# Kernel tuning notes

Measured on AMD Instinct MI355X. Metric: run time of the kernel, lower is better.

## Reference

```python
import jax, jax.numpy as jnp
import numpy as np

N_TOKENS = 131072      # flattened batch of latents
EMBED_DIM = 64         # embedding_dim
NUM_CODES = 1024       # num_embeddings
COMMIT_COST = 0.25     # commitment_cost
EPS_NORM = 1e-12       # F.normalize eps


def _l2_normalize(x):
    # matches F.normalize(x, dim=1): x / max(||x||_2, eps)
    n = jnp.sqrt(jnp.sum(x * x, axis=1, keepdims=True))
    return x / jnp.maximum(n, EPS_NORM)


def setup_inputs() -> dict:
    key = jax.random.key(0)
    k_in, k_w = jax.random.split(key)
    inputs = jax.random.normal(k_in, (N_TOKENS, EMBED_DIM), dtype=jnp.float32)
    # codebook init: uniform(-1/K, 1/K), as in the torch module
    weight = jax.random.uniform(k_w, (NUM_CODES, EMBED_DIM), dtype=jnp.float32,
                                minval=-1.0 / NUM_CODES, maxval=1.0 / NUM_CODES)
    return {"inputs": inputs, "weight": weight}


def reference(inputs, weight):
    # Eval-mode forward of VectorQuantizer (EMA/anchor update is a training-only
    # in-place buffer mutation and is excluded from the functional reference).
    input_shape = inputs.shape
    d = weight.shape[1]
    flat = inputs.reshape(-1, d)                         # [N, D]

    normed_z = _l2_normalize(jax.lax.stop_gradient(flat))  # [N, D]
    normed_cb = _l2_normalize(weight)                       # [K, D]
    # distances = -cosine similarity; argmin picks closest code
    distances = -jnp.einsum('nd,kd->nk', normed_z, normed_cb)  # [N, K]
    idx = jnp.argmin(distances, axis=1)                         # [N]

    encodings = jax.nn.one_hot(idx, weight.shape[0], dtype=jnp.float32)  # [N, K]
    # one-hot @ weight == gather of codebook rows
    quantized = jnp.take(weight, idx, axis=0).reshape(input_shape)

    e_latent_loss = jnp.mean((jax.lax.stop_gradient(quantized) - inputs) ** 2)
    q_latent_loss = jnp.mean((quantized - jax.lax.stop_gradient(inputs)) ** 2)
    loss = q_latent_loss + COMMIT_COST * e_latent_loss

    # straight-through estimator
    quantized_st = inputs + jax.lax.stop_gradient(quantized - inputs)

    avg_probs = jnp.mean(encodings, axis=0)  # [K]
    perplexity = jnp.exp(-jnp.sum(avg_probs * jnp.log(avg_probs + 1e-10)))

    return loss, quantized_st, perplexity, encodings
```

## Files before the change

### kernel.cpp

```cpp
#include <hip/hip_runtime.h>
#include <math.h>

#define N_TOK 131072
#define DIM 64
#define KCODES 1024
#define TPB 128
#define TIE_EPS 1e-4f

typedef __attribute__((ext_vector_type(8))) short short8;
typedef __attribute__((ext_vector_type(4))) float float4v;

static __device__ inline unsigned short f2bf(float x) {
    unsigned u = __float_as_uint(x);
    unsigned r = (u + 0x7FFF + ((u >> 16) & 1)) >> 16;
    return (unsigned short)r;
}
static __device__ inline float bf2f(unsigned short b) {
    return __uint_as_float(((unsigned)b) << 16);
}

__global__ __launch_bounds__(64) void vq_prep(
    const float* __restrict__ w, unsigned short* __restrict__ bfrag_hi,
    unsigned short* __restrict__ bfrag_lo, double* __restrict__ inv_n64,
    float* __restrict__ nw, int* __restrict__ count, int* __restrict__ nflag,
    double* __restrict__ delta)
{
    int k = blockIdx.x;
    int d = threadIdx.x;
    float v = w[k * DIM + d];
    float s = v * v;
    #pragma unroll
    for (int off = 32; off; off >>= 1) s += __shfl_xor(s, off);
    float den = fmaxf(sqrtf(s), 1e-12f);
    float nv = v / den;
    unsigned short hi = f2bf(nv);
    unsigned short lo = f2bf(nv - bf2f(hi));

    int t  = k >> 4;
    int nl = k & 15;
    int s2 = d >> 5;
    int q  = (d >> 3) & 3;
    int j  = d & 7;
    int l  = nl + 16 * q;
    size_t pos = ((size_t)(t * 2 + s2) * 64 + l) * 8 + j;
    bfrag_hi[pos] = hi;
    bfrag_lo[pos] = lo;

    double vd = (double)v;
    double sd = vd * vd;
    #pragma unroll
    for (int off = 32; off; off >>= 1) sd += __shfl_xor(sd, off);
    if (d == 0) {
        inv_n64[k] = 1.0 / fmax(sqrt(sd), 1e-12);
        nw[k] = den;
    }
    if (k == 0) {
        for (int i = d; i < KCODES; i += 64) count[i] = 0;
        if (d == 0) { nflag[0] = 0; delta[0] = 0.0; }
    }
}

static __device__ inline void merge3(float& b, float& s, int& i, float ob, float os, int oi) {
    if (ob > b) { s = fmaxf(b, os); b = ob; i = oi; }
    else if (ob == b) { s = b; if (oi < i) i = oi; }
    else { s = fmaxf(s, ob); }
}

__global__ __launch_bounds__(256, 3) void vq_main(
    const float* __restrict__ inputs, const float* __restrict__ w,
    const unsigned short* __restrict__ bfrag_hi, const unsigned short* __restrict__ bfrag_lo,
    const float* __restrict__ nw, int* __restrict__ g_idx, int* __restrict__ count,
    double* __restrict__ partial, int* __restrict__ nflag, int* __restrict__ flags,
    float* __restrict__ out_q, float* __restrict__ out_enc)
{
    __shared__ int   s_idx[TPB];
    __shared__ float s_part[4];

    const int tid  = threadIdx.x;
    const int lane = tid & 63;
    const int wv   = tid >> 6;
    const int col  = lane & 15;
    const int quad = lane >> 4;
    const int n0   = blockIdx.x * TPB;

    short8 ah[2][2], al[2][2];
    float n2z[2];
    #pragma unroll
    for (int s = 0; s < 2; s++) {
        int m = n0 + wv * 32 + s * 16 + col;
        const float* zp = inputs + (size_t)m * DIM + quad * 8;
        float4 f0 = *(const float4*)zp;
        float4 f1 = *(const float4*)(zp + 4);
        float4 f2 = *(const float4*)(zp + 32);
        float4 f3 = *(const float4*)(zp + 36);
        float v[16] = {f0.x,f0.y,f0.z,f0.w, f1.x,f1.y,f1.z,f1.w,
                       f2.x,f2.y,f2.z,f2.w, f3.x,f3.y,f3.z,f3.w};
        float ss = 0.f;
        #pragma unroll
        for (int j = 0; j < 16; j++) ss += v[j] * v[j];
        ss += __shfl_xor(ss, 16);
        ss += __shfl_xor(ss, 32);
        n2z[s] = ss;
        float inv = 1.0f / fmaxf(sqrtf(ss), 1e-12f);
        #pragma unroll
        for (int j = 0; j < 8; j++) {
            float x0 = v[j] * inv;
            unsigned short h0 = f2bf(x0);
            ah[s][0][j] = (short)h0;
            al[s][0][j] = (short)f2bf(x0 - bf2f(h0));
            float x1 = v[8 + j] * inv;
            unsigned short h1 = f2bf(x1);
            ah[s][1][j] = (short)h1;
            al[s][1][j] = (short)f2bf(x1 - bf2f(h1));
        }
    }

    float best[8], sec[8]; int bidx[8];
    #pragma unroll
    for (int i = 0; i < 8; i++) { best[i] = -1e30f; sec[i] = -1e30f; bidx[i] = 0x7fffffff; }

    const short8* bhp = (const short8*)bfrag_hi;
    const short8* blp = (const short8*)bfrag_lo;
    short8 c0h = bhp[lane], c1h = bhp[64 + lane];
    short8 c0l = blp[lane], c1l = blp[64 + lane];

    for (int t = 0; t < 64; t++) {
        int tn = (t < 63) ? (t + 1) : 63;
        size_t o = (size_t)(2 * tn) * 64 + lane;
        short8 p0h = bhp[o], p1h = bhp[o + 64];
        short8 p0l = blp[o], p1l = blp[o + 64];

        float4v acc0 = {0.f,0.f,0.f,0.f}, acc1 = {0.f,0.f,0.f,0.f};
        acc0 = __builtin_amdgcn_mfma_f32_16x16x32_bf16(ah[0][0], c0h, acc0, 0,0,0);
        acc1 = __builtin_amdgcn_mfma_f32_16x16x32_bf16(ah[1][0], c0h, acc1, 0,0,0);
        acc0 = __builtin_amdgcn_mfma_f32_16x16x32_bf16(al[0][0], c0h, acc0, 0,0,0);
        acc1 = __builtin_amdgcn_mfma_f32_16x16x32_bf16(al[1][0], c0h, acc1, 0,0,0);
        acc0 = __builtin_amdgcn_mfma_f32_16x16x32_bf16(ah[0][0], c0l, acc0, 0,0,0);
        acc1 = __builtin_amdgcn_mfma_f32_16x16x32_bf16(ah[1][0], c0l, acc1, 0,0,0);
        acc0 = __builtin_amdgcn_mfma_f32_16x16x32_bf16(ah[0][1], c1h, acc0, 0,0,0);
        acc1 = __builtin_amdgcn_mfma_f32_16x16x32_bf16(ah[1][1], c1h, acc1, 0,0,0);
        acc0 = __builtin_amdgcn_mfma_f32_16x16x32_bf16(al[0][1], c1h, acc0, 0,0,0);
        acc1 = __builtin_amdgcn_mfma_f32_16x16x32_bf16(al[1][1], c1h, acc1, 0,0,0);
        acc0 = __builtin_amdgcn_mfma_f32_16x16x32_bf16(ah[0][1], c1l, acc0, 0,0,0);
        acc1 = __builtin_amdgcn_mfma_f32_16x16x32_bf16(ah[1][1], c1l, acc1, 0,0,0);

        int k = t * 16 + col;
        #pragma unroll
        for (int i = 0; i < 4; i++) {
            float v0 = acc0[i];
            bool g0 = v0 > best[i];
            sec[i]  = fmaxf(sec[i], fminf(v0, best[i]));
            best[i] = fmaxf(best[i], v0);
            bidx[i] = g0 ? k : bidx[i];
            float v1 = acc1[i];
            bool g1 = v1 > best[4 + i];
            sec[4 + i]  = fmaxf(sec[4 + i], fminf(v1, best[4 + i]));
            best[4 + i] = fmaxf(best[4 + i], v1);
            bidx[4 + i] = g1 ? k : bidx[4 + i];
        }
        c0h = p0h; c1h = p1h; c0l = p0l; c1l = p1l;
    }

    #pragma unroll
    for (int off = 1; off < 16; off <<= 1) {
        #pragma unroll
        for (int i = 0; i < 8; i++) {
            float ob = __shfl_xor(best[i], off);
            float os = __shfl_xor(sec[i], off);
            int   oi = __shfl_xor(bidx[i], off);
            merge3(best[i], sec[i], bidx[i], ob, os, oi);
        }
    }

    float lsum = 0.f;
    #pragma unroll
    for (int s = 0; s < 2; s++) {
        #pragma unroll
        for (int i = 0; i < 4; i++) {
            int r = s * 4 + i;
            float n2 = __shfl(n2z[s], quad * 4 + i);
            if (col == 0) {
                int u  = quad * 4 + i;
                int tl = wv * 32 + s * 16 + u;
                int k  = bidx[r];
                s_idx[tl] = k;
                g_idx[n0 + tl] = k;
                atomicAdd(&count[k], 1);
                if (best[r] - sec[r] < TIE_EPS) {
                    int p = atomicAdd(nflag, 1);
                    flags[p] = n0 + tl;
                }
                float nwk = nw[k];
                float zw  = best[r] * sqrtf(n2) * nwk;
                lsum += n2 - 2.f * zw + nwk * nwk;
            }
        }
    }
    lsum += __shfl_xor(lsum, 16);
    lsum += __shfl_xor(lsum, 32);
    if (lane == 0) s_part[wv] = lsum;
    __syncthreads();
    if (tid == 0)
        partial[blockIdx.x] = (double)(s_part[0] + s_part[1] + s_part[2] + s_part[3]);

    const size_t qbase = (size_t)n0 * DIM;
    #pragma unroll 4
    for (int i2 = 0; i2 < 32; i2++) {
        int p = i2 * 256 + tid;
        int r = p >> 6, c = p & 63;
        int k = s_idx[r];
        out_q[qbase + p] = w[(size_t)k * DIM + c];
    }
    float* erow = out_enc + (size_t)(n0 + wv * 32) * KCODES + lane * 2;
    #pragma unroll 2
    for (int r = 0; r < 32; r++) {
        int k = s_idx[wv * 32 + r];
        #pragma unroll
        for (int j = 0; j < 8; j++) {
            int c2 = j * 128 + lane * 2;
            float2 v;
            v.x = (c2     == k) ? 1.f : 0.f;
            v.y = (c2 + 1 == k) ? 1.f : 0.f;
            *(float2*)(erow + j * 128 - lane * 2 + lane * 2) = v;
        }
        erow += KCODES;
    }
}

__global__ __launch_bounds__(64) void vq_rescan(
    const float* __restrict__ inputs, const float* __restrict__ w,
    const double* __restrict__ inv_n64, const int* __restrict__ g_idx,
    const int* __restrict__ flags, const int* __restrict__ nflag,
    int* __restrict__ count, float* __restrict__ out_q,
    float* __restrict__ out_enc, double* __restrict__ delta)
{
    __shared__ double sz[64];
    int lane = threadIdx.x;
    int nf = nflag[0];
    for (int i = blockIdx.x; i < nf; i += gridDim.x) {
        int tok = flags[i];
        double zd = (double)inputs[(size_t)tok * DIM + lane];
        double ss = zd * zd;
        #pragma unroll
        for (int off = 32; off; off >>= 1) ss += __shfl_xor(ss, off);
        sz[lane] = zd / fmax(sqrt(ss), 1e-12);
        __syncthreads();
        double bv = -1e300; int bi = 0x7fffffff;
        for (int c = 0; c < 16; c++) {
            int k = c * 64 + lane;
            double invk = inv_n64[k];
            double dot = 0.0;
            #pragma unroll 8
            for (int d = 0; d < DIM; d++)
                dot += sz[d] * ((double)w[(size_t)k * DIM + d] * invk);
            if (dot > bv) { bv = dot; bi = k; }
        }
        #pragma unroll
        for (int off = 1; off < 64; off <<= 1) {
            double ov = __shfl_xor(bv, off);
            int   oi = __shfl_xor(bi, off);
            if (ov > bv || (ov == bv && oi < bi)) { bv = ov; bi = oi; }
        }
        int kold = g_idx[tok];
        if (bi != kold) {
            double wn = (double)w[(size_t)bi * DIM + lane];
            double wo = (double)w[(size_t)kold * DIM + lane];
            double zr = (double)inputs[(size_t)tok * DIM + lane];
            double a = wn * wn - wo * wo - 2.0 * zr * (wn - wo);
            #pragma unroll
            for (int off = 32; off; off >>= 1) a += __shfl_xor(a, off);
            out_q[(size_t)tok * DIM + lane] = (float)wn;
            if (lane == 0) {
                atomicAdd(&count[kold], -1);
                atomicAdd(&count[bi], 1);
                out_enc[(size_t)tok * KCODES + kold] = 0.f;
                out_enc[(size_t)tok * KCODES + bi]   = 1.f;
                atomicAdd(delta, a);
            }
        }
        __syncthreads();
    }
}

__global__ __launch_bounds__(256) void vq_final(
    const int* __restrict__ count, const double* __restrict__ partial,
    const double* __restrict__ delta, float* __restrict__ out_loss,
    float* __restrict__ out_perp)
{
    __shared__ double s1[256], s2[256];
    int tid = threadIdx.x;
    double lp = 0.0, ls = 0.0;
    for (int k = tid; k < KCODES; k += 256) {
        double p = (double)count[k] / (double)N_TOK;
        lp += p * log(p + 1e-10);
    }
    for (int i = tid; i < 1024; i += 256) ls += partial[i];
    s1[tid] = lp; s2[tid] = ls;
    __syncthreads();
    for (int st = 128; st; st >>= 1) {
        if (tid < st) { s1[tid] += s1[tid + st]; s2[tid] += s2[tid + st]; }
        __syncthreads();
    }
    if (tid == 0) {
        out_perp[0] = (float)exp(-s1[0]);
        out_loss[0] = (float)(1.25 * (s2[0] + delta[0]) / ((double)N_TOK * (double)DIM));
    }
}

extern "C" void kernel_launch(void* const* d_in, const int* in_sizes, int n_in,
                              void* d_out, int out_size, void* d_ws, size_t ws_size,
                              hipStream_t stream) {
    const float* inputs = (const float*)d_in[0];
    const float* weight = (const float*)d_in[1];
    float* out      = (float*)d_out;
    float* out_loss = out;
    float* out_q    = out + 1;
    float* out_perp = out + 1 + (size_t)N_TOK * DIM;
    float* out_enc  = out_perp + 1;

    char* ws = (char*)d_ws;
    unsigned short* bfrag_hi = (unsigned short*)ws;
    unsigned short* bfrag_lo = (unsigned short*)(ws + 131072);
    double* inv_n64 = (double*)(ws + 262144);
    float*  nw      = (float*)(ws + 270336);
    int*    g_idx   = (int*)(ws + 274432);
    int*    count   = (int*)(ws + 798720);
    double* partial = (double*)(ws + 802816);
    double* delta   = (double*)(ws + 811008);
    int*    nflag   = (int*)(ws + 811016);
    int*    flags   = (int*)(ws + 811020);

    vq_prep<<<KCODES, 64, 0, stream>>>(weight, bfrag_hi, bfrag_lo, inv_n64, nw,
                                       count, nflag, delta);
    vq_main<<<N_TOK / TPB, 256, 0, stream>>>(inputs, weight, bfrag_hi, bfrag_lo, nw,
                                             g_idx, count, partial, nflag, flags,
                                             out_q, out_enc);
    vq_rescan<<<256, 64, 0, stream>>>(inputs, weight, inv_n64, g_idx, flags, nflag,
                                      count, out_q, out_enc, delta);
    vq_final<<<1, 256, 0, stream>>>(count, partial, delta, out_loss, out_perp);
}
```

Baseline: 692.9 us.

## Interleave one-hot zero-fill with distance loop and scatter ones afterward

Moves the zero-fill of the block's encodings tile into the MFMA codebook loop, so the large output stores overlap with matrix compute instead of running as a separate tail phase. The ones are then written with a single scatter store per token once the argmin indices are known. The second-best tracking is also reduced to a single fmed3 instruction, and launch bounds are raised to four blocks per SIMD. The risks are register pressure from the higher occupancy target and ordering between the zero stores and the later one-store. The odd offset of 2 also makes the float4 stores only 8-byte aligned.

```diff
diff --git a/kernel.cpp b/kernel.cpp
--- a/kernel.cpp
+++ b/kernel.cpp
@@ -66,7 +66,7 @@
     else { s = fmaxf(s, ob); }
 }
 
-__global__ __launch_bounds__(256, 3) void vq_main(
+__global__ __launch_bounds__(256, 4) void vq_main(
     const float* __restrict__ inputs, const float* __restrict__ w,
     const unsigned short* __restrict__ bfrag_hi, const unsigned short* __restrict__ bfrag_lo,
     const float* __restrict__ nw, int* __restrict__ g_idx, int* __restrict__ count,
@@ -115,6 +115,10 @@
         }
     }
 
+    float* enc0 = out_enc + (size_t)n0 * KCODES;
+    float* zp4  = enc0 + 2 + tid * 4;
+    const float4 zero4 = {0.f, 0.f, 0.f, 0.f};
+
     float best[8], sec[8]; int bidx[8];
     #pragma unroll
     for (int i = 0; i < 8; i++) { best[i] = -1e30f; sec[i] = -1e30f; bidx[i] = 0x7fffffff; }
@@ -129,6 +133,12 @@
         size_t o = (size_t)(2 * tn) * 64 + lane;
         short8 p0h = bhp[o], p1h = bhp[o + 64];
         short8 p0l = blp[o], p1l = blp[o + 64];
+
+        if (t < 63) {
+            *(float4*)zp4 = zero4;
+            *(float4*)(zp4 + KCODES) = zero4;
+            zp4 += 2 * KCODES;
+        }
 
         float4v acc0 = {0.f,0.f,0.f,0.f}, acc1 = {0.f,0.f,0.f,0.f};
         acc0 = __builtin_amdgcn_mfma_f32_16x16x32_bf16(ah[0][0], c0h, acc0, 0,0,0);
@@ -148,17 +158,27 @@
         #pragma unroll
         for (int i = 0; i < 4; i++) {
             float v0 = acc0[i];
+            sec[i]  = __builtin_amdgcn_fmed3f(best[i], sec[i], v0);
             bool g0 = v0 > best[i];
-            sec[i]  = fmaxf(sec[i], fminf(v0, best[i]));
             best[i] = fmaxf(best[i], v0);
             bidx[i] = g0 ? k : bidx[i];
             float v1 = acc1[i];
+            sec[4+i]  = __builtin_amdgcn_fmed3f(best[4+i], sec[4+i], v1);
             bool g1 = v1 > best[4 + i];
-            sec[4 + i]  = fmaxf(sec[4 + i], fminf(v1, best[4 + i]));
             best[4 + i] = fmaxf(best[4 + i], v1);
             bidx[4 + i] = g1 ? k : bidx[4 + i];
         }
         c0h = p0h; c1h = p1h; c0l = p0l; c1l = p1l;
+    }
+
+    #pragma unroll
+    for (int i = 126; i < 128; i++) {
+        int q = i * 256 + tid;
+        if (q < 32767) *(float4*)(enc0 + 2 + 4 * (size_t)q) = zero4;
+    }
+    if (tid == 0) {
+        *(float2*)enc0 = make_float2(0.f, 0.f);
+        *(float2*)(enc0 + (size_t)TPB * KCODES - 2) = make_float2(0.f, 0.f);
     }
 
     #pragma unroll
@@ -203,6 +223,9 @@
     if (tid == 0)
         partial[blockIdx.x] = (double)(s_part[0] + s_part[1] + s_part[2] + s_part[3]);
 
+    if (tid < TPB)
+        out_enc[(size_t)(n0 + tid) * KCODES + s_idx[tid]] = 1.0f;
+
     const size_t qbase = (size_t)n0 * DIM;
     #pragma unroll 4
     for (int i2 = 0; i2 < 32; i2++) {
@@ -210,20 +233,6 @@
         int r = p >> 6, c = p & 63;
         int k = s_idx[r];
         out_q[qbase + p] = w[(size_t)k * DIM + c];
-    }
-    float* erow = out_enc + (size_t)(n0 + wv * 32) * KCODES + lane * 2;
-    #pragma unroll 2
-    for (int r = 0; r < 32; r++) {
-        int k = s_idx[wv * 32 + r];
-        #pragma unroll
-        for (int j = 0; j < 8; j++) {
-            int c2 = j * 128 + lane * 2;
-            float2 v;
-            v.x = (c2     == k) ? 1.f : 0.f;
-            v.y = (c2 + 1 == k) ? 1.f : 0.f;
-            *(float2*)(erow + j * 128 - lane * 2 + lane * 2) = v;
-        }
-        erow += KCODES;
     }
 }
 
```

Measured after the change: 679.4 us. About the same (-1.9%).
